# Performance work log

Hardware: AMD Instinct MI355X
Metric: run time of the kernel (lower is better)

The kernel has to match this reference:

```python
import jax, jax.numpy as jnp
import numpy as np

GROUPS = 32
EPS = 1e-5


def setup_inputs() -> dict:
    key = jax.random.key(0)
    ks = jax.random.split(key, 6)
    B, H, W, C = 4, 64, 64, 512
    s = 1.0 / np.sqrt(C)
    return {
        "x": jax.random.normal(ks[0], (B, H, W, C), dtype=jnp.float32),
        "gamma": jnp.ones((C,), jnp.float32),
        "beta": jnp.zeros((C,), jnp.float32),
        "wq": jax.random.normal(ks[1], (C, C), jnp.float32) * s,
        "bq": jnp.zeros((C,), jnp.float32),
        "wk": jax.random.normal(ks[2], (C, C), jnp.float32) * s,
        "bk": jnp.zeros((C,), jnp.float32),
        "wv": jax.random.normal(ks[3], (C, C), jnp.float32) * s,
        "bv": jnp.zeros((C,), jnp.float32),
        "wp": jax.random.normal(ks[4], (C, C), jnp.float32) * s,
        "bp": jnp.zeros((C,), jnp.float32),
    }


def _group_norm(x, gamma, beta):
    B, H, W, C = x.shape
    cg = C // GROUPS
    xg = x.reshape(B, H, W, GROUPS, cg)
    mu = jnp.mean(xg, axis=(1, 2, 4), keepdims=True)
    var = jnp.var(xg, axis=(1, 2, 4), keepdims=True)
    xn = ((xg - mu) * jax.lax.rsqrt(var + EPS)).reshape(B, H, W, C)
    return xn * gamma + beta


def reference(x, gamma, beta, wq, bq, wk, bk, wv, bv, wp, bp):
    B, H, W, C = x.shape
    N = H * W
    xn = _group_norm(x, gamma, beta)
    # 1x1 convs == channel-wise dense layers
    q = (xn @ wq + bq).reshape(B, N, C)
    k = (xn @ wk + bk).reshape(B, N, C)
    v = (xn @ wv + bv).reshape(B, N, C)
    scores = jnp.einsum("bic,bjc->bij", q, k) * (C ** -0.5)  # [B, N, N]
    attn = jax.nn.softmax(scores, axis=-1)
    out = jnp.einsum("bij,bjc->bic", attn, v).reshape(B, H, W, C)
    return out @ wp + bp + x
```

## Files before the change

### kernel.cpp

```cpp
#include <hip/hip_runtime.h>
#include <hip/hip_bf16.h>

typedef __attribute__((ext_vector_type(4))) float f32x4;
typedef __attribute__((ext_vector_type(8))) short s16x8;
typedef unsigned short ushort_t;

#define N_DIM 4096
#define C_DIM 512

static __device__ __forceinline__ unsigned short f2bf(float f) {
    union { float f; unsigned u; } v; v.f = f;
    unsigned r = v.u + 0x7FFFu + ((v.u >> 16) & 1u);
    return (unsigned short)(r >> 16);
}
static __device__ __forceinline__ float bf2f(unsigned short u) {
    union { unsigned u; float f; } v; v.u = ((unsigned)u) << 16;
    return v.f;
}

__global__ void gn_stats_kernel(const float* __restrict__ x, float* __restrict__ stats) {
    int bg = blockIdx.x;
    int b = bg >> 5, g = bg & 31;
    const float* base = x + (size_t)b * (N_DIM * C_DIM) + g * 16;
    float sum = 0.f, ss = 0.f;
    for (int n = threadIdx.x; n < N_DIM; n += 256) {
        const float4* p = (const float4*)(base + (size_t)n * C_DIM);
        #pragma unroll
        for (int t = 0; t < 4; ++t) {
            float4 v = p[t];
            sum += v.x + v.y + v.z + v.w;
            ss  += v.x*v.x + v.y*v.y + v.z*v.z + v.w*v.w;
        }
    }
    #pragma unroll
    for (int o = 32; o > 0; o >>= 1) {
        sum += __shfl_down(sum, o);
        ss  += __shfl_down(ss, o);
    }
    __shared__ float red[8];
    int wid = threadIdx.x >> 6, lane = threadIdx.x & 63;
    if (lane == 0) { red[wid*2] = sum; red[wid*2+1] = ss; }
    __syncthreads();
    if (threadIdx.x == 0) {
        sum = red[0]+red[2]+red[4]+red[6];
        ss  = red[1]+red[3]+red[5]+red[7];
        float mean = sum * (1.f/65536.f);
        float var  = ss  * (1.f/65536.f) - mean*mean;
        stats[bg*2]   = mean;
        stats[bg*2+1] = rsqrtf(var + 1e-5f);
    }
}

__global__ void gn_norm_kernel(const float* __restrict__ x, const float* __restrict__ gamma,
                               const float* __restrict__ beta, const float* __restrict__ stats,
                               ushort_t* __restrict__ xn) {
    size_t i = ((size_t)blockIdx.x * 256 + threadIdx.x) * 4;
    int c = (int)(i & 511);
    int b = (int)(i >> 21);
    int bg = b*32 + (c >> 4);
    float mean = stats[bg*2], rstd = stats[bg*2+1];
    float4 v  = *(const float4*)(x + i);
    float4 ga = *(const float4*)(gamma + c);
    float4 be = *(const float4*)(beta + c);
    ushort4 o;
    o.x = f2bf((v.x - mean) * rstd * ga.x + be.x);
    o.y = f2bf((v.y - mean) * rstd * ga.y + be.y);
    o.z = f2bf((v.z - mean) * rstd * ga.z + be.z);
    o.w = f2bf((v.w - mean) * rstd * ga.w + be.w);
    *(ushort4*)(xn + i) = o;
}

__global__ void wconv_kernel(const float* __restrict__ wq, const float* __restrict__ wk,
                             const float* __restrict__ wv, const float* __restrict__ wp,
                             ushort_t* __restrict__ wt) {
    int idx = blockIdx.x * 256 + threadIdx.x;
    int m = idx >> 18;
    int r = idx & 262143;
    int ci = r >> 9, co = r & 511;
    const float* w = (m == 0) ? wq : (m == 1) ? wk : (m == 2) ? wv : wp;
    wt[(size_t)m * 262144 + (size_t)co * 512 + ci] = f2bf(w[(size_t)ci * 512 + co]);
}

__global__ __launch_bounds__(256) void qkv_kernel(const ushort_t* __restrict__ xn, const ushort_t* __restrict__ wt,
                         const float* __restrict__ bq, const float* __restrict__ bk, const float* __restrict__ bv,
                         ushort_t* __restrict__ q, ushort_t* __restrict__ k, ushort_t* __restrict__ v) {
    __shared__ char alds[2][8192];
    __shared__ char blds[2][8192];
    const int tid = threadIdx.x;
    const int w = tid >> 6, lane = tid & 63;
    const int lr = lane & 15, lg = lane >> 4;
    const int wr = w >> 1, wc = w & 1;
    const int m0 = blockIdx.x * 128;
    const int c0g = blockIdx.y * 128;
    const int z = c0g >> 9;
    const int c0 = c0g & 511;
    const ushort_t* W = wt + (size_t)z * 262144;
    const float* bias = (z == 0) ? bq : (z == 1) ? bk : bv;
    const float scale = (z == 0) ? 0.04419417382415922f : 1.0f;

    f32x4 acc[4][4];
    #pragma unroll
    for (int a = 0; a < 4; ++a)
        #pragma unroll
        for (int b = 0; b < 4; ++b) acc[a][b] = (f32x4){0.f,0.f,0.f,0.f};

    const int g1 = tid, g2 = tid + 256;
    const int r1 = g1 >> 2, s1 = ((g1 & 3) ^ (r1 & 3)) << 4;
    const int r2g = g2 >> 2, s2 = ((g2 & 3) ^ (r2g & 3)) << 4;

    auto STAGE = [&](int buf, int k0) {
        const char* A = (const char*)xn + (size_t)(m0) * 1024 + k0 * 2;
        const char* B = (const char*)W + (size_t)(c0) * 1024 + k0 * 2;
        __builtin_amdgcn_global_load_lds((const __attribute__((address_space(1))) void*)(A + (size_t)r1 * 1024 + s1),
            (__attribute__((address_space(3))) void*)(&alds[buf][g1 * 16]), 16, 0, 0);
        __builtin_amdgcn_global_load_lds((const __attribute__((address_space(1))) void*)(A + (size_t)r2g * 1024 + s2),
            (__attribute__((address_space(3))) void*)(&alds[buf][g2 * 16]), 16, 0, 0);
        __builtin_amdgcn_global_load_lds((const __attribute__((address_space(1))) void*)(B + (size_t)r1 * 1024 + s1),
            (__attribute__((address_space(3))) void*)(&blds[buf][g1 * 16]), 16, 0, 0);
        __builtin_amdgcn_global_load_lds((const __attribute__((address_space(1))) void*)(B + (size_t)r2g * 1024 + s2),
            (__attribute__((address_space(3))) void*)(&blds[buf][g2 * 16]), 16, 0, 0);
    };

    STAGE(0, 0);
    for (int ks = 0; ks < 16; ++ks) {
        const int cur = ks & 1;
        if (ks < 15) {
            STAGE(cur ^ 1, (ks + 1) * 32);
            asm volatile("s_waitcnt vmcnt(4)" ::: "memory");
        } else {
            asm volatile("s_waitcnt vmcnt(0)" ::: "memory");
        }
        __builtin_amdgcn_s_barrier();
        asm volatile("" ::: "memory");
        s16x8 af[4], bf[4];
        #pragma unroll
        for (int mi = 0; mi < 4; ++mi) {
            int row = wr * 64 + mi * 16 + lr;
            af[mi] = *(const s16x8*)(&alds[cur][row * 64 + ((lg ^ (lr & 3)) << 4)]);
        }
        #pragma unroll
        for (int ni = 0; ni < 4; ++ni) {
            int row = wc * 64 + ni * 16 + lr;
            bf[ni] = *(const s16x8*)(&blds[cur][row * 64 + ((lg ^ (lr & 3)) << 4)]);
        }
        #pragma unroll
        for (int mi = 0; mi < 4; ++mi)
            #pragma unroll
            for (int ni = 0; ni < 4; ++ni)
                acc[mi][ni] = __builtin_amdgcn_mfma_f32_16x16x32_bf16(af[mi], bf[ni], acc[mi][ni], 0, 0, 0);
        asm volatile("" ::: "memory");
        __builtin_amdgcn_s_barrier();
    }

    if (z < 2) {
        ushort_t* out = (z == 0) ? q : k;
        #pragma unroll
        for (int ni = 0; ni < 4; ++ni) {
            int cg = c0 + wc * 64 + ni * 16 + lr;
            float bb = bias[cg];
            #pragma unroll
            for (int mi = 0; mi < 4; ++mi) {
                int row = m0 + wr * 64 + mi * 16 + lg * 4;
                #pragma unroll
                for (int r2 = 0; r2 < 4; ++r2)
                    out[(size_t)(row + r2) * 512 + cg] = f2bf((acc[mi][ni][r2] + bb) * scale);
            }
        }
    } else {
        #pragma unroll
        for (int ni = 0; ni < 4; ++ni) {
            int cg = c0 + wc * 64 + ni * 16 + lr;
            float bb = bias[cg];
            #pragma unroll
            for (int mi = 0; mi < 4; ++mi) {
                int row = m0 + wr * 64 + mi * 16 + lg * 4;
                int batch = row >> 12, j = row & 4095;
                ushort4 o;
                o.x = f2bf(acc[mi][ni][0] + bb);
                o.y = f2bf(acc[mi][ni][1] + bb);
                o.z = f2bf(acc[mi][ni][2] + bb);
                o.w = f2bf(acc[mi][ni][3] + bb);
                *(ushort4*)(v + (size_t)batch * (512*4096) + (size_t)cg * 4096 + j) = o;
            }
        }
    }
}

__global__ __launch_bounds__(256) void attn_kernel(const ushort_t* __restrict__ q, const ushort_t* __restrict__ k,
                          const ushort_t* __restrict__ vt, ushort_t* __restrict__ Op0,
                          ushort_t* __restrict__ Op1, float2* __restrict__ stats2) {
    __shared__ char slds[131072 + 4096 + 256];
    char* plds = slds + 131072;
    float* rlds = (float*)(slds + 131072 + 4096);
    const int tid = threadIdx.x;
    const int w = tid >> 6, lane = tid & 63;
    const int lr = lane & 15, lg = lane >> 4;
    const int batch = blockIdx.y;
    const int js = blockIdx.z;
    const int i0 = blockIdx.x * 64;
    const int jbase = js * 2048;
    const char* kb = (const char*)(k  + (size_t)batch * (4096 * 512));
    const char* vb = (const char*)(vt + (size_t)batch * (512 * 4096));
    const ushort_t* qb = q + (size_t)batch * (4096 * 512);

    s16x8 qf[16];
    {
        const ushort_t* qrow = qb + (size_t)(i0 + w * 16 + lr) * 512 + lg * 8;
        #pragma unroll
        for (int t = 0; t < 16; ++t) qf[t] = *(const s16x8*)(qrow + t * 32);
    }

    f32x4 acc[8][4];
    #pragma unroll
    for (int a = 0; a < 8; ++a)
        #pragma unroll
        for (int b = 0; b < 4; ++b) acc[a][b] = (f32x4){0.f,0.f,0.f,0.f};
    float m = -1e30f, s = 0.f;

    const int vswz = ((lane & 3) ^ ((lane >> 3) & 3)) << 4;

    auto STAGE = [&](int buf, int j0) {
        char* lb = slds + buf * 65536;
        const char* gk = kb + (size_t)j0 * 1024;
        #pragma unroll
        for (int r = 0; r < 8; ++r) {
            int row = w * 8 + r;
            __builtin_amdgcn_global_load_lds(
                (const __attribute__((address_space(1))) void*)(gk + (size_t)row * 1024 + ((lane ^ r) << 4)),
                (__attribute__((address_space(3))) void*)(lb + row * 1024), 16, 0, 0);
        }
        const char* gv = vb + (size_t)j0 * 2;
        char* lv = lb + 32768;
        #pragma unroll
        for (int r = 0; r < 8; ++r) {
            int p = w * 8 + r;
            int c = p * 16 + (lane >> 2);
            __builtin_amdgcn_global_load_lds(
                (const __attribute__((address_space(1))) void*)(gv + (size_t)c * 8192 + vswz),
                (__attribute__((address_space(3))) void*)(lv + p * 1024), 16, 0, 0);
        }
    };

    STAGE(0, jbase);

    for (int t = 0; t < 64; ++t) {
        const int cur = t & 1;
        if (t < 63) {
            STAGE(cur ^ 1, jbase + (t + 1) * 32);
            asm volatile("s_waitcnt vmcnt(16)" ::: "memory");
        } else {
            asm volatile("s_waitcnt vmcnt(0)" ::: "memory");
        }
        __builtin_amdgcn_s_barrier();
        asm volatile("" ::: "memory");

        const char* kl = slds + cur * 65536;
        const char* vl = kl + 32768;

        f32x4 sa = {0,0,0,0}, sb = {0,0,0,0}, sc2 = {0,0,0,0}, sd = {0,0,0,0};
        #pragma unroll
        for (int tt = 0; tt < 16; tt += 2) {
            s16x8 k0f = *(const s16x8*)(kl + lr * 1024        + ((tt*64 + lg*16)     ^ ((lr&7)*16)));
            s16x8 k1f = *(const s16x8*)(kl + lr * 1024        + (((tt+1)*64 + lg*16) ^ ((lr&7)*16)));
            s16x8 k2f = *(const s16x8*)(kl + (16+lr) * 1024   + ((tt*64 + lg*16)     ^ ((lr&7)*16)));
            s16x8 k3f = *(const s16x8*)(kl + (16+lr) * 1024   + (((tt+1)*64 + lg*16) ^ ((lr&7)*16)));
            sa  = __builtin_amdgcn_mfma_f32_16x16x32_bf16(k0f, qf[tt],   sa,  0,0,0);
            sb  = __builtin_amdgcn_mfma_f32_16x16x32_bf16(k1f, qf[tt+1], sb,  0,0,0);
            sc2 = __builtin_amdgcn_mfma_f32_16x16x32_bf16(k2f, qf[tt],   sc2, 0,0,0);
            sd  = __builtin_amdgcn_mfma_f32_16x16x32_bf16(k3f, qf[tt+1], sd,  0,0,0);
        }
        f32x4 s1 = sa + sb;
        f32x4 s2 = sc2 + sd;

        float tm = fmaxf(fmaxf(fmaxf(s1[0], s1[1]), fmaxf(s1[2], s1[3])),
                         fmaxf(fmaxf(s2[0], s2[1]), fmaxf(s2[2], s2[3])));
        tm = fmaxf(tm, __shfl_xor(tm, 16));
        tm = fmaxf(tm, __shfl_xor(tm, 32));
        float resc = 1.f;
        if (!__all(tm <= m + 8.f)) {
            float mnew = fmaxf(m, tm);
            resc = __expf(m - mnew);
            s *= resc;
            m = mnew;
        }
        f32x4 p1, p2;
        #pragma unroll
        for (int r2 = 0; r2 < 4; ++r2) { p1[r2] = __expf(s1[r2] - m); p2[r2] = __expf(s2[r2] - m); }
        float ts = p1[0]+p1[1]+p1[2]+p1[3] + p2[0]+p2[1]+p2[2]+p2[3];
        ts += __shfl_xor(ts, 16);
        ts += __shfl_xor(ts, 32);
        s += ts;

        {
            unsigned w0 = (unsigned)f2bf(p1[0]) | ((unsigned)f2bf(p1[1]) << 16);
            unsigned w1 = (unsigned)f2bf(p1[2]) | ((unsigned)f2bf(p1[3]) << 16);
            unsigned w2 = (unsigned)f2bf(p2[0]) | ((unsigned)f2bf(p2[1]) << 16);
            unsigned w3 = (unsigned)f2bf(p2[2]) | ((unsigned)f2bf(p2[3]) << 16);
            char* prow = plds + w * 1024 + lr * 64 + ((lg & 1) << 3);
            *(uint2*)(prow + ((((lg >> 1)    ) ^ (lr & 3)) << 4)) = (uint2){w0, w1};
            *(uint2*)(prow + (((2 | (lg >> 1)) ^ (lr & 3)) << 4)) = (uint2){w2, w3};
            if (lg == 0) rlds[w * 16 + lr] = resc;
        }
        asm volatile("s_waitcnt lgkmcnt(0)" ::: "memory");
        __builtin_amdgcn_s_barrier();
        asm volatile("" ::: "memory");

        {
            float rf0 = rlds[lr], rf1 = rlds[16 + lr], rf2 = rlds[32 + lr], rf3 = rlds[48 + lr];
            if (__any(rf0 != 1.f || rf1 != 1.f || rf2 != 1.f || rf3 != 1.f)) {
                #pragma unroll
                for (int ct = 0; ct < 8; ++ct) {
                    acc[ct][0] *= rf0; acc[ct][1] *= rf1; acc[ct][2] *= rf2; acc[ct][3] *= rf3;
                }
            }
        }
        s16x8 pf[4];
        #pragma unroll
        for (int g = 0; g < 4; ++g)
            pf[g] = *(const s16x8*)(plds + g * 1024 + lr * 64 + ((lg ^ (lr & 3)) << 4));

        #pragma unroll
        for (int ct = 0; ct < 8; ++ct) {
            int c = w * 128 + ct * 16 + lr;
            s16x8 vf = *(const s16x8*)(vl + c * 64 + ((lg ^ ((lr >> 1) & 3)) << 4));
            #pragma unroll
            for (int g = 0; g < 4; ++g)
                acc[ct][g] = __builtin_amdgcn_mfma_f32_16x16x32_bf16(vf, pf[g], acc[ct][g], 0,0,0);
        }
        asm volatile("" ::: "memory");
        __builtin_amdgcn_s_barrier();
    }

    if (lg == 0) {
        rlds[w * 16 + lr] = 1.f / s;
        stats2[((size_t)(batch * 2 + js)) * 4096 + i0 + w * 16 + lr] = (float2){m, s};
    }
    __syncthreads();
    ushort_t* Op = js ? Op1 : Op0;
    float inv0 = rlds[lr], inv1 = rlds[16 + lr], inv2 = rlds[32 + lr], inv3 = rlds[48 + lr];
    #pragma unroll
    for (int ct = 0; ct < 8; ++ct) {
        #pragma unroll
        for (int g = 0; g < 4; ++g) {
            float iv = (g == 0) ? inv0 : (g == 1) ? inv1 : (g == 2) ? inv2 : inv3;
            ushort4 o;
            o.x = f2bf(acc[ct][g][0] * iv);
            o.y = f2bf(acc[ct][g][1] * iv);
            o.z = f2bf(acc[ct][g][2] * iv);
            o.w = f2bf(acc[ct][g][3] * iv);
            *(ushort4*)(Op + ((size_t)batch * 4096 + i0 + g*16 + lr) * 512
                        + w * 128 + ct * 16 + lg * 4) = o;
        }
    }
}

__global__ void combine_kernel(ushort_t* __restrict__ Op0, const ushort_t* __restrict__ Op1,
                               const float2* __restrict__ stats2) {
    int idx = blockIdx.x * 256 + threadIdx.x;
    int row = idx >> 7;
    int cc = (idx & 127) << 2;
    int b = row >> 12, r = row & 4095;
    float2 st0 = stats2[((size_t)(b * 2 + 0)) * 4096 + r];
    float2 st1 = stats2[((size_t)(b * 2 + 1)) * 4096 + r];
    float M = fmaxf(st0.x, st1.x);
    float w0 = __expf(st0.x - M) * st0.y;
    float w1 = __expf(st1.x - M) * st1.y;
    float rden = 1.f / (w0 + w1);
    w0 *= rden; w1 *= rden;
    size_t off = (size_t)row * 512 + cc;
    ushort4 a = *(ushort4*)(Op0 + off);
    ushort4 c4 = *(const ushort4*)(Op1 + off);
    ushort4 o;
    o.x = f2bf(w0 * bf2f(a.x) + w1 * bf2f(c4.x));
    o.y = f2bf(w0 * bf2f(a.y) + w1 * bf2f(c4.y));
    o.z = f2bf(w0 * bf2f(a.z) + w1 * bf2f(c4.z));
    o.w = f2bf(w0 * bf2f(a.w) + w1 * bf2f(c4.w));
    *(ushort4*)(Op0 + off) = o;
}

__global__ __launch_bounds__(256) void proj_kernel(const ushort_t* __restrict__ O, const ushort_t* __restrict__ wt,
                          const float* __restrict__ bp, const float* __restrict__ x, float* __restrict__ out) {
    __shared__ char alds[2][8192];
    __shared__ char blds[2][8192];
    const int tid = threadIdx.x;
    const int w = tid >> 6, lane = tid & 63;
    const int lr = lane & 15, lg = lane >> 4;
    const int wr = w >> 1, wc = w & 1;
    const int m0 = blockIdx.x * 128;
    const int c0 = blockIdx.y * 128;
    const ushort_t* W = wt + (size_t)3 * 262144;

    f32x4 acc[4][4];
    #pragma unroll
    for (int a = 0; a < 4; ++a)
        #pragma unroll
        for (int b = 0; b < 4; ++b) acc[a][b] = (f32x4){0.f,0.f,0.f,0.f};

    const int g1 = tid, g2 = tid + 256;
    const int r1 = g1 >> 2, s1 = ((g1 & 3) ^ (r1 & 3)) << 4;
    const int r2g = g2 >> 2, s2 = ((g2 & 3) ^ (r2g & 3)) << 4;

    auto STAGE = [&](int buf, int k0) {
        const char* A = (const char*)O + (size_t)(m0) * 1024 + k0 * 2;
        const char* B = (const char*)W + (size_t)(c0) * 1024 + k0 * 2;
        __builtin_amdgcn_global_load_lds((const __attribute__((address_space(1))) void*)(A + (size_t)r1 * 1024 + s1),
            (__attribute__((address_space(3))) void*)(&alds[buf][g1 * 16]), 16, 0, 0);
        __builtin_amdgcn_global_load_lds((const __attribute__((address_space(1))) void*)(A + (size_t)r2g * 1024 + s2),
            (__attribute__((address_space(3))) void*)(&alds[buf][g2 * 16]), 16, 0, 0);
        __builtin_amdgcn_global_load_lds((const __attribute__((address_space(1))) void*)(B + (size_t)r1 * 1024 + s1),
            (__attribute__((address_space(3))) void*)(&blds[buf][g1 * 16]), 16, 0, 0);
        __builtin_amdgcn_global_load_lds((const __attribute__((address_space(1))) void*)(B + (size_t)r2g * 1024 + s2),
            (__attribute__((address_space(3))) void*)(&blds[buf][g2 * 16]), 16, 0, 0);
    };

    STAGE(0, 0);
    for (int ks = 0; ks < 16; ++ks) {
        const int cur = ks & 1;
        if (ks < 15) {
            STAGE(cur ^ 1, (ks + 1) * 32);
            asm volatile("s_waitcnt vmcnt(4)" ::: "memory");
        } else {
            asm volatile("s_waitcnt vmcnt(0)" ::: "memory");
        }
        __builtin_amdgcn_s_barrier();
        asm volatile("" ::: "memory");
        s16x8 af[4], bf[4];
        #pragma unroll
        for (int mi = 0; mi < 4; ++mi) {
            int row = wr * 64 + mi * 16 + lr;
            af[mi] = *(const s16x8*)(&alds[cur][row * 64 + ((lg ^ (lr & 3)) << 4)]);
        }
        #pragma unroll
        for (int ni = 0; ni < 4; ++ni) {
            int row = wc * 64 + ni * 16 + lr;
            bf[ni] = *(const s16x8*)(&blds[cur][row * 64 + ((lg ^ (lr & 3)) << 4)]);
        }
        #pragma unroll
        for (int mi = 0; mi < 4; ++mi)
            #pragma unroll
            for (int ni = 0; ni < 4; ++ni)
                acc[mi][ni] = __builtin_amdgcn_mfma_f32_16x16x32_bf16(af[mi], bf[ni], acc[mi][ni], 0, 0, 0);
        asm volatile("" ::: "memory");
        __builtin_amdgcn_s_barrier();
    }

    #pragma unroll
    for (int ni = 0; ni < 4; ++ni) {
        int cg = c0 + wc * 64 + ni * 16 + lr;
        float bb = bp[cg];
        #pragma unroll
        for (int mi = 0; mi < 4; ++mi) {
            int row = m0 + wr * 64 + mi * 16 + lg * 4;
            #pragma unroll
            for (int r2 = 0; r2 < 4; ++r2) {
                size_t idx = (size_t)(row + r2) * 512 + cg;
                out[idx] = acc[mi][ni][r2] + bb + x[idx];
            }
        }
    }
}

extern "C" void kernel_launch(void* const* d_in, const int* in_sizes, int n_in,
                              void* d_out, int out_size, void* d_ws, size_t ws_size,
                              hipStream_t stream) {
    (void)in_sizes; (void)n_in; (void)out_size; (void)ws_size;
    const float* x     = (const float*)d_in[0];
    const float* gamma = (const float*)d_in[1];
    const float* beta  = (const float*)d_in[2];
    const float* wq    = (const float*)d_in[3];
    const float* bq    = (const float*)d_in[4];
    const float* wk    = (const float*)d_in[5];
    const float* bk    = (const float*)d_in[6];
    const float* wv    = (const float*)d_in[7];
    const float* bv    = (const float*)d_in[8];
    const float* wp    = (const float*)d_in[9];
    const float* bp    = (const float*)d_in[10];
    float* out = (float*)d_out;

    char* ws = (char*)d_ws;
    ushort_t* wt    = (ushort_t*)(ws);
    float*    stats = (float*)(ws + (2ull<<20));
    float2*   st2   = (float2*)(ws + (3ull<<20));
    ushort_t* xn    = (ushort_t*)(ws + (4ull<<20));
    ushort_t* qb    = (ushort_t*)(ws + (20ull<<20));
    ushort_t* kb    = (ushort_t*)(ws + (36ull<<20));
    ushort_t* vt    = (ushort_t*)(ws + (52ull<<20));
    ushort_t* Ob    = (ushort_t*)(ws + (68ull<<20));

    hipLaunchKernelGGL(wconv_kernel,    dim3(4096),       dim3(256), 0, stream, wq, wk, wv, wp, wt);
    hipLaunchKernelGGL(gn_stats_kernel, dim3(128),        dim3(256), 0, stream, x, stats);
    hipLaunchKernelGGL(gn_norm_kernel,  dim3(8192),       dim3(256), 0, stream, x, gamma, beta, stats, xn);
    hipLaunchKernelGGL(qkv_kernel,      dim3(128, 12),    dim3(256), 0, stream, xn, wt, bq, bk, bv, qb, kb, vt);
    hipLaunchKernelGGL(attn_kernel,     dim3(64, 4, 2),   dim3(256), 0, stream, qb, kb, vt, Ob, xn, st2);
    hipLaunchKernelGGL(combine_kernel,  dim3(8192),       dim3(256), 0, stream, Ob, xn, st2);
    hipLaunchKernelGGL(proj_kernel,     dim3(128, 4),     dim3(256), 0, stream, Ob, wt, bp, x, out);
}
```

Baseline: 393.6 us.

## Split attention output channels across blocks, drop double-buffering for higher occupancy

The attention kernel now splits the 512 value channels into two halves across grid.z, so each block accumulates only 256 output channels. That halves the accumulator registers and V staging. LDS drops from about 132KB to about 53KB and waves_per_eu(2) is requested, so more blocks can be resident. In exchange, QK^T scores and softmax are computed twice, once per channel half, and the K/V double-buffer prefetch is removed, so each iteration waits synchronously on its loads. The intent is to rely on occupancy rather than software pipelining to hide latency.

```diff
diff --git a/kernel.cpp b/kernel.cpp
--- a/kernel.cpp
+++ b/kernel.cpp
@@ -186,21 +186,24 @@
     }
 }
 
-__global__ __launch_bounds__(256) void attn_kernel(const ushort_t* __restrict__ q, const ushort_t* __restrict__ k,
-                          const ushort_t* __restrict__ vt, ushort_t* __restrict__ Op0,
-                          ushort_t* __restrict__ Op1, float2* __restrict__ stats2) {
-    __shared__ char slds[131072 + 4096 + 256];
-    char* plds = slds + 131072;
-    float* rlds = (float*)(slds + 131072 + 4096);
+__global__ __launch_bounds__(256) __attribute__((amdgpu_waves_per_eu(2)))
+void attn_kernel(const ushort_t* __restrict__ q, const ushort_t* __restrict__ k,
+                 const ushort_t* __restrict__ vt, ushort_t* __restrict__ Op0,
+                 ushort_t* __restrict__ Op1, float2* __restrict__ stats2) {
+    __shared__ char slds[32768 + 16384 + 4096 + 256];
+    char* vlds = slds + 32768;
+    char* plds = slds + 32768 + 16384;
+    float* rlds = (float*)(slds + 32768 + 16384 + 4096);
     const int tid = threadIdx.x;
     const int w = tid >> 6, lane = tid & 63;
     const int lr = lane & 15, lg = lane >> 4;
     const int batch = blockIdx.y;
-    const int js = blockIdx.z;
+    const int js = blockIdx.z >> 1;
+    const int ch = blockIdx.z & 1;
     const int i0 = blockIdx.x * 64;
     const int jbase = js * 2048;
     const char* kb = (const char*)(k  + (size_t)batch * (4096 * 512));
-    const char* vb = (const char*)(vt + (size_t)batch * (512 * 4096));
+    const char* vb = (const char*)(vt + (size_t)batch * (512 * 4096) + (size_t)ch * 256 * 4096);
     const ushort_t* qb = q + (size_t)batch * (4096 * 512);
 
     s16x8 qf[16];
@@ -210,67 +213,51 @@
         for (int t = 0; t < 16; ++t) qf[t] = *(const s16x8*)(qrow + t * 32);
     }
 
-    f32x4 acc[8][4];
-    #pragma unroll
-    for (int a = 0; a < 8; ++a)
+    f32x4 acc[4][4];
+    #pragma unroll
+    for (int a = 0; a < 4; ++a)
         #pragma unroll
         for (int b = 0; b < 4; ++b) acc[a][b] = (f32x4){0.f,0.f,0.f,0.f};
     float m = -1e30f, s = 0.f;
 
     const int vswz = ((lane & 3) ^ ((lane >> 3) & 3)) << 4;
 
-    auto STAGE = [&](int buf, int j0) {
-        char* lb = slds + buf * 65536;
+    auto STAGE = [&](int j0) {
         const char* gk = kb + (size_t)j0 * 1024;
         #pragma unroll
         for (int r = 0; r < 8; ++r) {
             int row = w * 8 + r;
             __builtin_amdgcn_global_load_lds(
                 (const __attribute__((address_space(1))) void*)(gk + (size_t)row * 1024 + ((lane ^ r) << 4)),
-                (__attribute__((address_space(3))) void*)(lb + row * 1024), 16, 0, 0);
+                (__attribute__((address_space(3))) void*)(slds + row * 1024), 16, 0, 0);
         }
         const char* gv = vb + (size_t)j0 * 2;
-        char* lv = lb + 32768;
-        #pragma unroll
-        for (int r = 0; r < 8; ++r) {
-            int p = w * 8 + r;
+        #pragma unroll
+        for (int r = 0; r < 4; ++r) {
+            int p = w * 4 + r;
             int c = p * 16 + (lane >> 2);
             __builtin_amdgcn_global_load_lds(
                 (const __attribute__((address_space(1))) void*)(gv + (size_t)c * 8192 + vswz),
-                (__attribute__((address_space(3))) void*)(lv + p * 1024), 16, 0, 0);
+                (__attribute__((address_space(3))) void*)(vlds + p * 1024), 16, 0, 0);
         }
     };
 
-    STAGE(0, jbase);
-
     for (int t = 0; t < 64; ++t) {
-        const int cur = t & 1;
-        if (t < 63) {
-            STAGE(cur ^ 1, jbase + (t + 1) * 32);
-            asm volatile("s_waitcnt vmcnt(16)" ::: "memory");
-        } else {
-            asm volatile("s_waitcnt vmcnt(0)" ::: "memory");
-        }
-        __builtin_amdgcn_s_barrier();
-        asm volatile("" ::: "memory");
-
-        const char* kl = slds + cur * 65536;
-        const char* vl = kl + 32768;
-
-        f32x4 sa = {0,0,0,0}, sb = {0,0,0,0}, sc2 = {0,0,0,0}, sd = {0,0,0,0};
-        #pragma unroll
-        for (int tt = 0; tt < 16; tt += 2) {
-            s16x8 k0f = *(const s16x8*)(kl + lr * 1024        + ((tt*64 + lg*16)     ^ ((lr&7)*16)));
-            s16x8 k1f = *(const s16x8*)(kl + lr * 1024        + (((tt+1)*64 + lg*16) ^ ((lr&7)*16)));
-            s16x8 k2f = *(const s16x8*)(kl + (16+lr) * 1024   + ((tt*64 + lg*16)     ^ ((lr&7)*16)));
-            s16x8 k3f = *(const s16x8*)(kl + (16+lr) * 1024   + (((tt+1)*64 + lg*16) ^ ((lr&7)*16)));
-            sa  = __builtin_amdgcn_mfma_f32_16x16x32_bf16(k0f, qf[tt],   sa,  0,0,0);
-            sb  = __builtin_amdgcn_mfma_f32_16x16x32_bf16(k1f, qf[tt+1], sb,  0,0,0);
-            sc2 = __builtin_amdgcn_mfma_f32_16x16x32_bf16(k2f, qf[tt],   sc2, 0,0,0);
-            sd  = __builtin_amdgcn_mfma_f32_16x16x32_bf16(k3f, qf[tt+1], sd,  0,0,0);
-        }
-        f32x4 s1 = sa + sb;
-        f32x4 s2 = sc2 + sd;
+        STAGE(jbase + t * 32);
+        asm volatile("s_waitcnt vmcnt(0)" ::: "memory");
+        __builtin_amdgcn_s_barrier();
+        asm volatile("" ::: "memory");
+
+        f32x4 sa = {0,0,0,0}, sb = {0,0,0,0};
+        #pragma unroll
+        for (int tt = 0; tt < 16; ++tt) {
+            s16x8 k0f = *(const s16x8*)(slds + lr * 1024        + ((tt*64 + lg*16) ^ ((lr&7)*16)));
+            s16x8 k2f = *(const s16x8*)(slds + (16+lr) * 1024   + ((tt*64 + lg*16) ^ ((lr&7)*16)));
+            sa = __builtin_amdgcn_mfma_f32_16x16x32_bf16(k0f, qf[tt], sa, 0,0,0);
+            sb = __builtin_amdgcn_mfma_f32_16x16x32_bf16(k2f, qf[tt], sb, 0,0,0);
+        }
+        f32x4 s1 = sa;
+        f32x4 s2 = sb;
 
         float tm = fmaxf(fmaxf(fmaxf(s1[0], s1[1]), fmaxf(s1[2], s1[3])),
                          fmaxf(fmaxf(s2[0], s2[1]), fmaxf(s2[2], s2[3])));
@@ -309,7 +296,7 @@
             float rf0 = rlds[lr], rf1 = rlds[16 + lr], rf2 = rlds[32 + lr], rf3 = rlds[48 + lr];
             if (__any(rf0 != 1.f || rf1 != 1.f || rf2 != 1.f || rf3 != 1.f)) {
                 #pragma unroll
-                for (int ct = 0; ct < 8; ++ct) {
+                for (int ct = 0; ct < 4; ++ct) {
                     acc[ct][0] *= rf0; acc[ct][1] *= rf1; acc[ct][2] *= rf2; acc[ct][3] *= rf3;
                 }
             }
@@ -320,9 +307,9 @@
             pf[g] = *(const s16x8*)(plds + g * 1024 + lr * 64 + ((lg ^ (lr & 3)) << 4));
 
         #pragma unroll
-        for (int ct = 0; ct < 8; ++ct) {
-            int c = w * 128 + ct * 16 + lr;
-            s16x8 vf = *(const s16x8*)(vl + c * 64 + ((lg ^ ((lr >> 1) & 3)) << 4));
+        for (int ct = 0; ct < 4; ++ct) {
+            int c = w * 64 + ct * 16 + lr;
+            s16x8 vf = *(const s16x8*)(vlds + c * 64 + ((lg ^ ((lr >> 1) & 3)) << 4));
             #pragma unroll
             for (int g = 0; g < 4; ++g)
                 acc[ct][g] = __builtin_amdgcn_mfma_f32_16x16x32_bf16(vf, pf[g], acc[ct][g], 0,0,0);
@@ -333,13 +320,14 @@
 
     if (lg == 0) {
         rlds[w * 16 + lr] = 1.f / s;
-        stats2[((size_t)(batch * 2 + js)) * 4096 + i0 + w * 16 + lr] = (float2){m, s};
+        if (ch == 0)
+            stats2[((size_t)(batch * 2 + js)) * 4096 + i0 + w * 16 + lr] = (float2){m, s};
     }
     __syncthreads();
     ushort_t* Op = js ? Op1 : Op0;
     float inv0 = rlds[lr], inv1 = rlds[16 + lr], inv2 = rlds[32 + lr], inv3 = rlds[48 + lr];
     #pragma unroll
-    for (int ct = 0; ct < 8; ++ct) {
+    for (int ct = 0; ct < 4; ++ct) {
         #pragma unroll
         for (int g = 0; g < 4; ++g) {
             float iv = (g == 0) ? inv0 : (g == 1) ? inv1 : (g == 2) ? inv2 : inv3;
@@ -349,7 +337,7 @@
             o.z = f2bf(acc[ct][g][2] * iv);
             o.w = f2bf(acc[ct][g][3] * iv);
             *(ushort4*)(Op + ((size_t)batch * 4096 + i0 + g*16 + lr) * 512
-                        + w * 128 + ct * 16 + lg * 4) = o;
+                        + ch * 256 + w * 64 + ct * 16 + lg * 4) = o;
         }
     }
 }
@@ -491,7 +479,7 @@
     hipLaunchKernelGGL(gn_stats_kernel, dim3(128),        dim3(256), 0, stream, x, stats);
     hipLaunchKernelGGL(gn_norm_kernel,  dim3(8192),       dim3(256), 0, stream, x, gamma, beta, stats, xn);
     hipLaunchKernelGGL(qkv_kernel,      dim3(128, 12),    dim3(256), 0, stream, xn, wt, bq, bk, bv, qb, kb, vt);
-    hipLaunchKernelGGL(attn_kernel,     dim3(64, 4, 2),   dim3(256), 0, stream, qb, kb, vt, Ob, xn, st2);
+    hipLaunchKernelGGL(attn_kernel,     dim3(64, 4, 4),   dim3(256), 0, stream, qb, kb, vt, Ob, xn, st2);
     hipLaunchKernelGGL(combine_kernel,  dim3(8192),       dim3(256), 0, stream, Ob, xn, st2);
     hipLaunchKernelGGL(proj_kernel,     dim3(128, 4),     dim3(256), 0, stream, Ob, wt, bp, x, out);
 }
```

Measured after the change: 406.4 us. +3.2%, slower.

## Software-pipeline attention loop: overlap next-tile QK softmax with current PV MMAs

Applied to the files above, without the earlier changes.

Splits K and V staging and restructures the flash-attention loop so the QK^T score and softmax for tile t+1 is computed right after the PV accumulation of tile t. P and rescale buffers are double-buffered in LDS. This cuts the loop from two barriers per iteration to one and lets score MFMAs interleave with PV MFMAs. In exchange the loop waits for vmcnt(0) every iteration, which gives up some global-load latency hiding, and LDS use grows slightly.

```diff
diff --git a/kernel.cpp b/kernel.cpp
--- a/kernel.cpp
+++ b/kernel.cpp
@@ -189,9 +189,9 @@
 __global__ __launch_bounds__(256) void attn_kernel(const ushort_t* __restrict__ q, const ushort_t* __restrict__ k,
                           const ushort_t* __restrict__ vt, ushort_t* __restrict__ Op0,
                           ushort_t* __restrict__ Op1, float2* __restrict__ stats2) {
-    __shared__ char slds[131072 + 4096 + 256];
+    __shared__ char slds[131072 + 8192 + 512];
     char* plds = slds + 131072;
-    float* rlds = (float*)(slds + 131072 + 4096);
+    float* rlds = (float*)(slds + 131072 + 8192);
     const int tid = threadIdx.x;
     const int w = tid >> 6, lane = tid & 63;
     const int lr = lane & 15, lg = lane >> 4;
@@ -219,7 +219,7 @@
 
     const int vswz = ((lane & 3) ^ ((lane >> 3) & 3)) << 4;
 
-    auto STAGE = [&](int buf, int j0) {
+    auto STAGE_K = [&](int buf, int j0) {
         char* lb = slds + buf * 65536;
         const char* gk = kb + (size_t)j0 * 1024;
         #pragma unroll
@@ -229,8 +229,10 @@
                 (const __attribute__((address_space(1))) void*)(gk + (size_t)row * 1024 + ((lane ^ r) << 4)),
                 (__attribute__((address_space(3))) void*)(lb + row * 1024), 16, 0, 0);
         }
+    };
+    auto STAGE_V = [&](int buf, int j0) {
+        char* lv = slds + buf * 65536 + 32768;
         const char* gv = vb + (size_t)j0 * 2;
-        char* lv = lb + 32768;
         #pragma unroll
         for (int r = 0; r < 8; ++r) {
             int p = w * 8 + r;
@@ -241,22 +243,8 @@
         }
     };
 
-    STAGE(0, jbase);
-
-    for (int t = 0; t < 64; ++t) {
-        const int cur = t & 1;
-        if (t < 63) {
-            STAGE(cur ^ 1, jbase + (t + 1) * 32);
-            asm volatile("s_waitcnt vmcnt(16)" ::: "memory");
-        } else {
-            asm volatile("s_waitcnt vmcnt(0)" ::: "memory");
-        }
-        __builtin_amdgcn_s_barrier();
-        asm volatile("" ::: "memory");
-
-        const char* kl = slds + cur * 65536;
-        const char* vl = kl + 32768;
-
+    auto QKSM = [&](int buf, int pbuf) {
+        const char* kl = slds + buf * 65536;
         f32x4 sa = {0,0,0,0}, sb = {0,0,0,0}, sc2 = {0,0,0,0}, sd = {0,0,0,0};
         #pragma unroll
         for (int tt = 0; tt < 16; tt += 2) {
@@ -291,22 +279,35 @@
         ts += __shfl_xor(ts, 32);
         s += ts;
 
+        unsigned w0 = (unsigned)f2bf(p1[0]) | ((unsigned)f2bf(p1[1]) << 16);
+        unsigned w1 = (unsigned)f2bf(p1[2]) | ((unsigned)f2bf(p1[3]) << 16);
+        unsigned w2 = (unsigned)f2bf(p2[0]) | ((unsigned)f2bf(p2[1]) << 16);
+        unsigned w3 = (unsigned)f2bf(p2[2]) | ((unsigned)f2bf(p2[3]) << 16);
+        char* prow = plds + pbuf * 4096 + w * 1024 + lr * 64 + ((lg & 1) << 3);
+        *(uint2*)(prow + ((((lg >> 1)    ) ^ (lr & 3)) << 4)) = (uint2){w0, w1};
+        *(uint2*)(prow + (((2 | (lg >> 1)) ^ (lr & 3)) << 4)) = (uint2){w2, w3};
+        if (lg == 0) rlds[pbuf * 64 + w * 16 + lr] = resc;
+    };
+
+    STAGE_K(0, jbase);
+    STAGE_V(0, jbase);
+    STAGE_K(1, jbase + 32);
+    asm volatile("s_waitcnt vmcnt(8)" ::: "memory");
+    __builtin_amdgcn_s_barrier();
+    asm volatile("" ::: "memory");
+    QKSM(0, 0);
+    asm volatile("s_waitcnt lgkmcnt(0)" ::: "memory");
+    __builtin_amdgcn_s_barrier();
+    asm volatile("" ::: "memory");
+
+    for (int t = 0; t < 64; ++t) {
+        const int cur = t & 1, nxt = cur ^ 1;
+        if (t < 62) STAGE_K(cur, jbase + (t + 2) * 32);
+        if (t < 63) STAGE_V(nxt, jbase + (t + 1) * 32);
+
         {
-            unsigned w0 = (unsigned)f2bf(p1[0]) | ((unsigned)f2bf(p1[1]) << 16);
-            unsigned w1 = (unsigned)f2bf(p1[2]) | ((unsigned)f2bf(p1[3]) << 16);
-            unsigned w2 = (unsigned)f2bf(p2[0]) | ((unsigned)f2bf(p2[1]) << 16);
-            unsigned w3 = (unsigned)f2bf(p2[2]) | ((unsigned)f2bf(p2[3]) << 16);
-            char* prow = plds + w * 1024 + lr * 64 + ((lg & 1) << 3);
-            *(uint2*)(prow + ((((lg >> 1)    ) ^ (lr & 3)) << 4)) = (uint2){w0, w1};
-            *(uint2*)(prow + (((2 | (lg >> 1)) ^ (lr & 3)) << 4)) = (uint2){w2, w3};
-            if (lg == 0) rlds[w * 16 + lr] = resc;
-        }
-        asm volatile("s_waitcnt lgkmcnt(0)" ::: "memory");
-        __builtin_amdgcn_s_barrier();
-        asm volatile("" ::: "memory");
-
-        {
-            float rf0 = rlds[lr], rf1 = rlds[16 + lr], rf2 = rlds[32 + lr], rf3 = rlds[48 + lr];
+            const float* rr = rlds + cur * 64;
+            float rf0 = rr[lr], rf1 = rr[16 + lr], rf2 = rr[32 + lr], rf3 = rr[48 + lr];
             if (__any(rf0 != 1.f || rf1 != 1.f || rf2 != 1.f || rf3 != 1.f)) {
                 #pragma unroll
                 for (int ct = 0; ct < 8; ++ct) {
@@ -317,8 +318,9 @@
         s16x8 pf[4];
         #pragma unroll
         for (int g = 0; g < 4; ++g)
-            pf[g] = *(const s16x8*)(plds + g * 1024 + lr * 64 + ((lg ^ (lr & 3)) << 4));
-
+            pf[g] = *(const s16x8*)(plds + cur * 4096 + g * 1024 + lr * 64 + ((lg ^ (lr & 3)) << 4));
+
+        const char* vl = slds + cur * 65536 + 32768;
         #pragma unroll
         for (int ct = 0; ct < 8; ++ct) {
             int c = w * 128 + ct * 16 + lr;
@@ -327,8 +329,12 @@
             for (int g = 0; g < 4; ++g)
                 acc[ct][g] = __builtin_amdgcn_mfma_f32_16x16x32_bf16(vf, pf[g], acc[ct][g], 0,0,0);
         }
+
+        if (t < 63) QKSM(nxt, nxt);
+
+        asm volatile("s_waitcnt vmcnt(0) lgkmcnt(0)" ::: "memory");
+        __builtin_amdgcn_s_barrier();
         asm volatile("" ::: "memory");
-        __builtin_amdgcn_s_barrier();
     }
 
     if (lg == 0) {
```

Result: faster. 359.1 us (-8.8%).
